# Performance work log

Measured on AMD Instinct MI355X. Metric: run time of the kernel, lower is better.

## Reference

```python
import jax, jax.numpy as jnp
import numpy as np

D_MODEL = 1024
B, S = 4, 4096


def setup_inputs() -> dict:
    key = jax.random.key(0)
    k1, k2, k3, k4, k5 = jax.random.split(key, 5)
    lim = 1.0 / np.sqrt(D_MODEL)  # nn.Linear default init range
    x = jax.random.normal(k1, (B, S, D_MODEL), dtype=jnp.float32)
    mask = jnp.ones((B, S), dtype=jnp.float32)
    W_up = jax.random.uniform(k2, (D_MODEL, D_MODEL), jnp.float32, -lim, lim)
    b_up = jax.random.uniform(k3, (D_MODEL,), jnp.float32, -lim, lim)
    W_f = jax.random.uniform(k4, (D_MODEL, D_MODEL), jnp.float32, -lim, lim)
    b_f = jax.random.uniform(k5, (D_MODEL,), jnp.float32, -lim, lim)
    decay_param = jnp.zeros((1,), dtype=jnp.float32)
    return {"x": x, "mask": mask, "W_up": W_up, "b_up": b_up,
            "W_f": W_f, "b_f": b_f, "decay_param": decay_param}


def _decay_scan(u, decay):
    # h_t = decay * h_{t-1} + u_t  along axis=1, via associative scan.
    # Element: (a, b) representing h -> a*h + b; compose: (a1*a2, b1*a2 + b2).
    a = jnp.broadcast_to(decay, u.shape)

    def combine(c1, c2):
        a1, b1 = c1
        a2, b2 = c2
        return a1 * a2, b1 * a2 + b2

    _, h = jax.lax.associative_scan(combine, (a, u), axis=1)
    return h


def reference(x, mask, W_up, b_up, W_f, b_f, decay_param):
    decay = jax.nn.sigmoid(decay_param)[0]
    # u_i = mask_i * linear_update(x_i)
    u = (jnp.einsum('bsd,ed->bse', x, W_up) + b_up) * mask[..., None]
    # h_t = sum_{i<=t} decay^(t-i) * u_i  (exponential-decay recurrence)
    h = _decay_scan(u, decay)
    return jnp.einsum('bsd,ed->bse', h, W_f) + b_f
```

## Files before the change

kernel.cpp:

```cpp
#include <hip/hip_runtime.h>
#include <hip/hip_bf16.h>
#include <cstdint>
#include <cstddef>

#define DMODEL 1024
#define BATCH  4
#define SEQ    4096
#define BSROWS (BATCH*SEQ)
#define CHUNK  32
#define NCHUNK (SEQ/CHUNK)
#define NCH_T  (BATCH*NCHUNK)

typedef __attribute__((ext_vector_type(8))) short bf16x8;
typedef __attribute__((ext_vector_type(4))) float f32x4;


__device__ __forceinline__ unsigned short f2bf(float f) {
  union { float f; uint32_t u; } v; v.f = f;
  uint32_t u = v.u;
  u += 0x7FFFu + ((u >> 16) & 1u);
  return (unsigned short)(u >> 16);
}

__device__ __forceinline__ float sigmoid_dev(const float* dp) {
  return 1.0f / (1.0f + expf(-dp[0]));
}

typedef __attribute__((address_space(1))) void void_g;
typedef __attribute__((address_space(3))) void void_l;

__device__ __forceinline__ void gl2lds16(const void* g, void* l) {
  __builtin_amdgcn_global_load_lds((void_g*)g, (void_l*)l, 16, 0, 0);
}

__device__ __forceinline__ void kloop64(
    const unsigned short* __restrict__ A, const unsigned short* __restrict__ B,
    int m0, int n0, f32x4 acc[2][2],
    unsigned short* As, unsigned short* Bs, int tid) {
  int lane = tid & 63, w = tid >> 6, wm = w & 1, wn = w >> 1;
  int quad = lane >> 4, l16 = lane & 15;
  int r = tid >> 3, cch = tid & 7;
  int g = cch ^ (r & 7);

  auto stage = [&](int t, int slot) {
    int k0 = t * 64;
    unsigned short* dA = As + slot * 4096;
    unsigned short* dB = Bs + slot * 4096;
    gl2lds16(A + (size_t)(m0 + r) * DMODEL + k0 + g * 8,      dA + r * 64 + cch * 8);
    gl2lds16(A + (size_t)(m0 + 32 + r) * DMODEL + k0 + g * 8, dA + (32 + r) * 64 + cch * 8);
    gl2lds16(B + (size_t)(n0 + r) * DMODEL + k0 + g * 8,      dB + r * 64 + cch * 8);
    gl2lds16(B + (size_t)(n0 + 32 + r) * DMODEL + k0 + g * 8, dB + (32 + r) * 64 + cch * 8);
  };
  auto compute = [&](int slot) {
    const bf16x8* Av = (const bf16x8*)(As + slot * 4096);
    const bf16x8* Bv = (const bf16x8*)(Bs + slot * 4096);
    #pragma unroll
    for (int kk = 0; kk < 2; ++kk) {
      bf16x8 af[2], bfr[2];
      #pragma unroll
      for (int i = 0; i < 2; ++i) {
        int rowA = wm * 32 + i * 16 + l16;
        af[i]  = Av[rowA * 8 + ((kk * 4 + quad) ^ (l16 & 7))];
        int rowB = wn * 32 + i * 16 + l16;
        bfr[i] = Bv[rowB * 8 + ((kk * 4 + quad) ^ (l16 & 7))];
      }
      __builtin_amdgcn_s_setprio(1);
      #pragma unroll
      for (int i = 0; i < 2; ++i)
        #pragma unroll
        for (int j = 0; j < 2; ++j)
          acc[i][j] = __builtin_amdgcn_mfma_f32_16x16x32_bf16(af[i], bfr[j], acc[i][j], 0, 0, 0);
      __builtin_amdgcn_s_setprio(0);
    }
  };

  stage(0, 0); stage(1, 1);
  asm volatile("s_waitcnt vmcnt(4)" ::: "memory");
  __builtin_amdgcn_s_barrier();
  asm volatile("" ::: "memory");
  int cur = 0;
  for (int t = 0; t < 14; ++t) {
    int ns = cur + 2; if (ns >= 3) ns -= 3;
    stage(t + 2, ns);
    compute(cur);
    asm volatile("s_waitcnt vmcnt(4)" ::: "memory");
    __builtin_amdgcn_s_barrier();
    asm volatile("" ::: "memory");
    cur = (cur == 2) ? 0 : cur + 1;
  }
  compute(cur);
  asm volatile("s_waitcnt vmcnt(0)" ::: "memory");
  __builtin_amdgcn_s_barrier();
  asm volatile("" ::: "memory");
  cur = (cur == 2) ? 0 : cur + 1;
  compute(cur);
}

__global__ __launch_bounds__(256) void prep_kernel(
    const float* __restrict__ x, const float* __restrict__ mask,
    const float* __restrict__ W_up, const float* __restrict__ b_up,
    const float* __restrict__ W_f, const float* __restrict__ dp,
    unsigned short* __restrict__ Wf_bf, unsigned short* __restrict__ WupT,
    float* __restrict__ bb, unsigned short* __restrict__ hv,
    float* __restrict__ carry, float* __restrict__ lbeta,
    float* __restrict__ cbeta) {
  __shared__ float tile[32][33];
  int blk = blockIdx.x;
  int tid = threadIdx.x;

  if (blk < 512) {
    float decay = sigmoid_dev(dp);
    int b = blk / NCHUNK, c = blk % NCHUNK;
    int base = b * SEQ + c * CHUNK;
    const float4* xp = (const float4*)(x + (size_t)base * DMODEL);
    const float4* mp4 = (const float4*)(mask + base);
    float mreg[32];
    #pragma unroll
    for (int q = 0; q < 8; ++q) {
      float4 t = mp4[q];
      mreg[q * 4 + 0] = t.x; mreg[q * 4 + 1] = t.y;
      mreg[q * 4 + 2] = t.z; mreg[q * 4 + 3] = t.w;
    }
    float4 h = make_float4(0.f, 0.f, 0.f, 0.f);
    #pragma unroll
    for (int s = 0; s < CHUNK; ++s) {
      float m = mreg[s];
      float4 xv = xp[(size_t)s * (DMODEL / 4) + tid];
      h.x = decay * h.x + m * xv.x;
      h.y = decay * h.y + m * xv.y;
      h.z = decay * h.z + m * xv.z;
      h.w = decay * h.w + m * xv.w;
      ushort4 o;
      o.x = f2bf(h.x); o.y = f2bf(h.y); o.z = f2bf(h.z); o.w = f2bf(h.w);
      ((ushort4*)hv)[(size_t)(base + s) * (DMODEL / 4) + tid] = o;
    }
    ((float4*)carry)[(size_t)blk * (DMODEL / 4) + tid] = h;
  } else if (blk < 1536) {
    int e = blk - 512;
    int lane = tid & 63, w = tid >> 6;
    float4 v = ((const float4*)(W_f + (size_t)e * DMODEL))[tid];
    float4 bu = ((const float4*)b_up)[tid];
    ushort4 o;
    o.x = f2bf(v.x); o.y = f2bf(v.y); o.z = f2bf(v.z); o.w = f2bf(v.w);
    ((ushort4*)(Wf_bf + (size_t)e * DMODEL))[tid] = o;
    float s = v.x * bu.x + v.y * bu.y + v.z * bu.z + v.w * bu.w;
    #pragma unroll
    for (int off = 32; off; off >>= 1) s += __shfl_down(s, off);
    if (lane == 0) ((float*)tile)[w] = s;
    __syncthreads();
    if (tid == 0)
      bb[e] = ((float*)tile)[0] + ((float*)tile)[1] +
              ((float*)tile)[2] + ((float*)tile)[3];
  } else if (blk < 2560) {
    int id = blk - 1536;
    int bx = id & 31, by = id >> 5;
    int tx = tid & 31, ty = tid >> 5;
    int xx = bx * 32 + tx;
    int y0 = by * 32;
    for (int j = ty; j < 32; j += 8)
      tile[j][tx] = W_up[(size_t)(y0 + j) * DMODEL + xx];
    __syncthreads();
    int dd = tid >> 3;
    int c4 = (tid & 7) * 4;
    ushort4 o;
    o.x = f2bf(tile[c4 + 0][dd]);
    o.y = f2bf(tile[c4 + 1][dd]);
    o.z = f2bf(tile[c4 + 2][dd]);
    o.w = f2bf(tile[c4 + 3][dd]);
    *(ushort4*)(WupT + (size_t)(bx * 32 + dd) * DMODEL + y0 + c4) = o;
  } else {
    float decay = sigmoid_dev(dp);
    int t = (blk - 2560) * 256 + tid;
    int s = t & 31;
    float h = mask[t];
    float wgt = decay;
    #pragma unroll
    for (int off = 1; off < 32; off <<= 1) {
      float up = __shfl_up(h, off);
      if (s >= off) h += wgt * up;
      wgt = wgt * wgt;
    }
    lbeta[t] = h;
    if (s == 31) cbeta[t >> 5] = h;
  }
}

__global__ __launch_bounds__(256) void mid2_kernel(
    const unsigned short* __restrict__ Wf_bf,
    const unsigned short* __restrict__ WupT,
    unsigned short* __restrict__ Wc,
    const float* __restrict__ carry, const float* __restrict__ cbeta,
    const float* __restrict__ dp,
    unsigned short* __restrict__ Pbf, float* __restrict__ pbeta) {
  __shared__ unsigned short As[3 * 64 * 64];
  __shared__ unsigned short Bs[3 * 64 * 64];
  int tid = threadIdx.x;
  if (blockIdx.x < 256) {
    int mt = blockIdx.x >> 4, nt = blockIdx.x & 15;
    f32x4 acc[2][2] = {};
    kloop64(Wf_bf, WupT, mt * 64, nt * 64, acc, As, Bs, tid);
    int lane = tid & 63, w = tid >> 6, wm = w & 1, wn = w >> 1;
    int quad = lane >> 4, l16 = lane & 15;
    #pragma unroll
    for (int j = 0; j < 2; ++j) {
      int col = nt * 64 + wn * 32 + j * 16 + l16;
      #pragma unroll
      for (int i = 0; i < 2; ++i) {
        int rowb = mt * 64 + wm * 32 + i * 16 + quad * 4;
        #pragma unroll
        for (int rr = 0; rr < 4; ++rr)
          Wc[(size_t)(rowb + rr) * DMODEL + col] = f2bf(acc[i][j][rr]);
      }
    }
  } else {
    float decay = sigmoid_dev(dp);
    float dL = powf(decay, (float)CHUNK);
    int gid = (blockIdx.x - 256) * 256 + tid;
    int b = gid >> 10, dd = gid & 1023;
    float P = 0.f;
    for (int c0 = 0; c0 < NCHUNK; c0 += 8) {
      float v[8];
      #pragma unroll
      for (int j = 0; j < 8; ++j)
        v[j] = carry[(size_t)(b * NCHUNK + c0 + j) * DMODEL + dd];
      #pragma unroll
      for (int j = 0; j < 8; ++j) {
        Pbf[(size_t)(b * NCHUNK + c0 + j) * DMODEL + dd] = f2bf(P);
        P = dL * P + v[j];
      }
    }
    if (dd == 0) {
      float Pb = 0.f;
      for (int c0 = 0; c0 < NCHUNK; c0 += 16) {
        float v[16];
        #pragma unroll
        for (int j = 0; j < 16; ++j) v[j] = cbeta[b * NCHUNK + c0 + j];
        #pragma unroll
        for (int j = 0; j < 16; ++j) {
          pbeta[b * NCHUNK + c0 + j] = Pb;
          Pb = dL * Pb + v[j];
        }
      }
    }
  }
}

__global__ __launch_bounds__(512) void gemm_main(
    const unsigned short* __restrict__ A,
    const unsigned short* __restrict__ Bm,
    const unsigned short* __restrict__ Pbf,
    const float* __restrict__ pbeta,
    const float* __restrict__ lbeta,
    const float* __restrict__ bb,
    const float* __restrict__ bias_f,
    const float* __restrict__ dp,
    float* __restrict__ out) {
  __shared__ unsigned short As[2 * 256 * 64];
  __shared__ unsigned short Bs[2 * 256 * 64];
  __shared__ unsigned short Ps[2 * 16 * 64];
  __shared__ float dpow[CHUNK];
  const int TSLOT = 256 * 64;
  const int PSLOT = 16 * 64;
  int tid = threadIdx.x;
  if (tid < CHUNK) {
    float decay = sigmoid_dev(dp);
    dpow[tid] = powf(decay, (float)(tid + 1));
  }

  int lane = tid & 63, wid = tid >> 6;
  int wm = wid >> 2, wn = wid & 3;
  int quad = lane >> 4, l16 = lane & 15;
  int r = tid >> 3, cch = tid & 7;
  int g = cch ^ (r & 7);

  int bid = blockIdx.x;
  int xcd = bid & 7, jb = bid >> 3;
  int m0 = (xcd * 8 + (jb >> 2)) * 256;
  int n0 = (jb & 3) * 256;
  int chunk0 = m0 >> 5;

  f32x4 acc[8][4] = {};
  f32x4 Pacc[4] = {};

  auto stageT = [&](int t, int p) {
    int k0 = t * 64;
    unsigned short* dA = As + p * TSLOT;
    unsigned short* dB = Bs + p * TSLOT;
    #pragma unroll
    for (int q = 0; q < 4; ++q)
      gl2lds16(A + (size_t)(m0 + q * 64 + r) * DMODEL + k0 + g * 8,
               dA + (q * 64 + r) * 64 + cch * 8);
    #pragma unroll
    for (int q = 0; q < 4; ++q)
      gl2lds16(Bm + (size_t)(n0 + q * 64 + r) * DMODEL + k0 + g * 8,
               dB + (q * 64 + r) * 64 + cch * 8);
    if (wid == 0) {
      int rp = lane >> 3, cp = lane & 7;
      int gp = cp ^ (rp & 7);
      gl2lds16(Pbf + (size_t)(chunk0 + rp) * DMODEL + k0 + gp * 8,
               Ps + p * PSLOT + lane * 8);
    }
  };
  auto compute = [&](int p) {
    const bf16x8* Av = (const bf16x8*)(As + p * TSLOT);
    const bf16x8* Bv = (const bf16x8*)(Bs + p * TSLOT);
    const bf16x8* Pv = (const bf16x8*)(Ps + p * PSLOT);
    #pragma unroll
    for (int kk = 0; kk < 2; ++kk) {
      bf16x8 bfr[4];
      #pragma unroll
      for (int j = 0; j < 4; ++j) {
        int rowB = wn * 64 + j * 16 + l16;
        bfr[j] = Bv[rowB * 8 + ((kk * 4 + quad) ^ (l16 & 7))];
      }
      bf16x8 pf = Pv[l16 * 8 + ((kk * 4 + quad) ^ (l16 & 7))];
      __builtin_amdgcn_s_setprio(1);
      #pragma unroll
      for (int j = 0; j < 4; ++j)
        Pacc[j] = __builtin_amdgcn_mfma_f32_16x16x32_bf16(pf, bfr[j], Pacc[j], 0, 0, 0);
      __builtin_amdgcn_s_setprio(0);
      #pragma unroll
      for (int i = 0; i < 8; ++i) {
        int rowA = wm * 128 + i * 16 + l16;
        bf16x8 af = Av[rowA * 8 + ((kk * 4 + quad) ^ (l16 & 7))];
        __builtin_amdgcn_s_setprio(1);
        #pragma unroll
        for (int j = 0; j < 4; ++j)
          acc[i][j] = __builtin_amdgcn_mfma_f32_16x16x32_bf16(af, bfr[j], acc[i][j], 0, 0, 0);
        __builtin_amdgcn_s_setprio(0);
      }
    }
  };

  stageT(0, 0);
  __syncthreads();

  for (int t = 0; t < 15; ++t) {
    int p = t & 1;
    stageT(t + 1, p ^ 1);
    compute(p);
    asm volatile("s_waitcnt vmcnt(0)" ::: "memory");
    __builtin_amdgcn_s_barrier();
    asm volatile("" ::: "memory");
  }
  compute(1);

  float* Plds = (float*)As;
  if (wm == 0 && quad < 2) {
    #pragma unroll
    for (int j = 0; j < 4; ++j)
      #pragma unroll
      for (int rr = 0; rr < 4; ++rr)
        Plds[(quad * 4 + rr) * 256 + wn * 64 + j * 16 + l16] = Pacc[j][rr];
  }
  __syncthreads();

  float bbv[4], bfv[4];
  #pragma unroll
  for (int j = 0; j < 4; ++j) {
    int col = n0 + wn * 64 + j * 16 + l16;
    bbv[j] = bb[col];
    bfv[j] = bias_f[col];
  }
  #pragma unroll
  for (int i = 0; i < 8; ++i) {
    int chl = wm * 4 + (i >> 1);
    float pb = pbeta[chunk0 + chl];
    #pragma unroll
    for (int rr = 0; rr < 4; ++rr) {
      int row = m0 + wm * 128 + i * 16 + quad * 4 + rr;
      float lb  = lbeta[row];
      float dpw = dpow[row & 31];
      float* outRow = out + (size_t)row * DMODEL;
      #pragma unroll
      for (int j = 0; j < 4; ++j) {
        int col = n0 + wn * 64 + j * 16 + l16;
        float po = Plds[chl * 256 + wn * 64 + j * 16 + l16] + pb * bbv[j];
        outRow[col] = acc[i][j][rr] + dpw * po + lb * bbv[j] + bfv[j];
      }
    }
  }
}


extern "C" void kernel_launch(void* const* d_in, const int* in_sizes, int n_in,
                              void* d_out, int out_size, void* d_ws, size_t ws_size,
                              hipStream_t stream) {
  const float* x    = (const float*)d_in[0];
  const float* mask = (const float*)d_in[1];
  const float* W_up = (const float*)d_in[2];
  const float* b_up = (const float*)d_in[3];
  const float* W_f  = (const float*)d_in[4];
  const float* b_f  = (const float*)d_in[5];
  const float* dp   = (const float*)d_in[6];
  float* out = (float*)d_out;

  char* ws = (char*)d_ws;
  unsigned short* hv    = (unsigned short*)(ws);
  unsigned short* Wc    = (unsigned short*)(ws + 33554432);
  unsigned short* Wf_bf = (unsigned short*)(ws + 35651584);
  unsigned short* WupT  = (unsigned short*)(ws + 37748736);
  float* carry  = (float*)(ws + 39845888);
  unsigned short* Pbf = (unsigned short*)(ws + 41943040);
  float* lbeta  = (float*)(ws + 45088768);
  float* cbeta  = (float*)(ws + 45154304);
  float* pbeta  = (float*)(ws + 45156352);
  float* bb     = (float*)(ws + 45158400);

  prep_kernel<<<2624, 256, 0, stream>>>(x, mask, W_up, b_up, W_f, dp,
                                        Wf_bf, WupT, bb, hv, carry, lbeta, cbeta);
  mid2_kernel<<<272, 256, 0, stream>>>(Wf_bf, WupT, Wc, carry, cbeta, dp,
                                       Pbf, pbeta);
  gemm_main<<<256, 512, 0, stream>>>(hv, Wc, Pbf, pbeta, lbeta, bb, b_f, dp, out);
}
```

Before: 185.3 us.

## Split prep kernel into scan and weight-prep kernels with x prefetch

The monolithic prep kernel is split into two launches. One handles the per-chunk decay scan and now computes the local beta prefix inline, removing the separate mask-scan blocks. The scan loop also software-prefetches x rows two steps ahead to keep more loads in flight. The W_f conversion now has each wave handle one row, which drops the shared-memory reduction and barrier; the cost is an extra kernel launch and a serial 32-step loop computing the beta values.

```diff
diff --git a/kernel.cpp b/kernel.cpp
--- a/kernel.cpp
+++ b/kernel.cpp
@@ -96,63 +96,88 @@
   compute(cur);
 }
 
-__global__ __launch_bounds__(256) void prep_kernel(
+__global__ __launch_bounds__(256) void prep_scan(
     const float* __restrict__ x, const float* __restrict__ mask,
+    const float* __restrict__ dp,
+    unsigned short* __restrict__ hv, float* __restrict__ carry,
+    float* __restrict__ lbeta, float* __restrict__ cbeta) {
+  int blk = blockIdx.x;
+  int tid = threadIdx.x;
+  float decay = sigmoid_dev(dp);
+  int b = blk / NCHUNK, c = blk % NCHUNK;
+  int base = b * SEQ + c * CHUNK;
+  const float4* xp = (const float4*)(x + (size_t)base * DMODEL);
+  const float4* mp4 = (const float4*)(mask + base);
+  float mreg[32];
+  #pragma unroll
+  for (int q = 0; q < 8; ++q) {
+    float4 t = mp4[q];
+    mreg[q * 4 + 0] = t.x; mreg[q * 4 + 1] = t.y;
+    mreg[q * 4 + 2] = t.z; mreg[q * 4 + 3] = t.w;
+  }
+
+  {
+    float hb = 0.f;
+    #pragma unroll
+    for (int i = 0; i < 32; ++i) {
+      float nv = decay * hb + mreg[i];
+      hb = (tid >= i) ? nv : hb;
+    }
+    if (tid < 32) {
+      lbeta[base + tid] = hb;
+      if (tid == 31) cbeta[base >> 5] = hb;
+    }
+  }
+
+  float4 x0 = xp[tid];
+  float4 x1 = xp[256 + tid];
+  float4 h = make_float4(0.f, 0.f, 0.f, 0.f);
+  #pragma unroll
+  for (int s = 0; s < CHUNK; ++s) {
+    float4 cur = x0;
+    x0 = x1;
+    if (s + 2 < CHUNK) x1 = xp[(size_t)(s + 2) * 256 + tid];
+    float m = mreg[s];
+    h.x = decay * h.x + m * cur.x;
+    h.y = decay * h.y + m * cur.y;
+    h.z = decay * h.z + m * cur.z;
+    h.w = decay * h.w + m * cur.w;
+    ushort4 o;
+    o.x = f2bf(h.x); o.y = f2bf(h.y); o.z = f2bf(h.z); o.w = f2bf(h.w);
+    ((ushort4*)hv)[(size_t)(base + s) * 256 + tid] = o;
+  }
+  ((float4*)carry)[(size_t)blk * 256 + tid] = h;
+}
+
+__global__ __launch_bounds__(256) void prep_misc(
     const float* __restrict__ W_up, const float* __restrict__ b_up,
-    const float* __restrict__ W_f, const float* __restrict__ dp,
+    const float* __restrict__ W_f,
     unsigned short* __restrict__ Wf_bf, unsigned short* __restrict__ WupT,
-    float* __restrict__ bb, unsigned short* __restrict__ hv,
-    float* __restrict__ carry, float* __restrict__ lbeta,
-    float* __restrict__ cbeta) {
+    float* __restrict__ bb) {
   __shared__ float tile[32][33];
   int blk = blockIdx.x;
   int tid = threadIdx.x;
-
-  if (blk < 512) {
-    float decay = sigmoid_dev(dp);
-    int b = blk / NCHUNK, c = blk % NCHUNK;
-    int base = b * SEQ + c * CHUNK;
-    const float4* xp = (const float4*)(x + (size_t)base * DMODEL);
-    const float4* mp4 = (const float4*)(mask + base);
-    float mreg[32];
-    #pragma unroll
-    for (int q = 0; q < 8; ++q) {
-      float4 t = mp4[q];
-      mreg[q * 4 + 0] = t.x; mreg[q * 4 + 1] = t.y;
-      mreg[q * 4 + 2] = t.z; mreg[q * 4 + 3] = t.w;
-    }
-    float4 h = make_float4(0.f, 0.f, 0.f, 0.f);
-    #pragma unroll
-    for (int s = 0; s < CHUNK; ++s) {
-      float m = mreg[s];
-      float4 xv = xp[(size_t)s * (DMODEL / 4) + tid];
-      h.x = decay * h.x + m * xv.x;
-      h.y = decay * h.y + m * xv.y;
-      h.z = decay * h.z + m * xv.z;
-      h.w = decay * h.w + m * xv.w;
+  if (blk < 256) {
+    int w = tid >> 6, lane = tid & 63;
+    int e = blk * 4 + w;
+    const float4* row4 = (const float4*)(W_f + (size_t)e * DMODEL);
+    const float4* bup4 = (const float4*)b_up;
+    ushort4* out4 = (ushort4*)(Wf_bf + (size_t)e * DMODEL);
+    float s = 0.f;
+    #pragma unroll
+    for (int q = 0; q < 4; ++q) {
+      float4 v  = row4[q * 64 + lane];
+      float4 bu = bup4[q * 64 + lane];
       ushort4 o;
-      o.x = f2bf(h.x); o.y = f2bf(h.y); o.z = f2bf(h.z); o.w = f2bf(h.w);
-      ((ushort4*)hv)[(size_t)(base + s) * (DMODEL / 4) + tid] = o;
-    }
-    ((float4*)carry)[(size_t)blk * (DMODEL / 4) + tid] = h;
-  } else if (blk < 1536) {
-    int e = blk - 512;
-    int lane = tid & 63, w = tid >> 6;
-    float4 v = ((const float4*)(W_f + (size_t)e * DMODEL))[tid];
-    float4 bu = ((const float4*)b_up)[tid];
-    ushort4 o;
-    o.x = f2bf(v.x); o.y = f2bf(v.y); o.z = f2bf(v.z); o.w = f2bf(v.w);
-    ((ushort4*)(Wf_bf + (size_t)e * DMODEL))[tid] = o;
-    float s = v.x * bu.x + v.y * bu.y + v.z * bu.z + v.w * bu.w;
+      o.x = f2bf(v.x); o.y = f2bf(v.y); o.z = f2bf(v.z); o.w = f2bf(v.w);
+      out4[q * 64 + lane] = o;
+      s += v.x * bu.x + v.y * bu.y + v.z * bu.z + v.w * bu.w;
+    }
     #pragma unroll
     for (int off = 32; off; off >>= 1) s += __shfl_down(s, off);
-    if (lane == 0) ((float*)tile)[w] = s;
-    __syncthreads();
-    if (tid == 0)
-      bb[e] = ((float*)tile)[0] + ((float*)tile)[1] +
-              ((float*)tile)[2] + ((float*)tile)[3];
-  } else if (blk < 2560) {
-    int id = blk - 1536;
+    if (lane == 0) bb[e] = s;
+  } else {
+    int id = blk - 256;
     int bx = id & 31, by = id >> 5;
     int tx = tid & 31, ty = tid >> 5;
     int xx = bx * 32 + tx;
@@ -168,20 +193,6 @@
     o.z = f2bf(tile[c4 + 2][dd]);
     o.w = f2bf(tile[c4 + 3][dd]);
     *(ushort4*)(WupT + (size_t)(bx * 32 + dd) * DMODEL + y0 + c4) = o;
-  } else {
-    float decay = sigmoid_dev(dp);
-    int t = (blk - 2560) * 256 + tid;
-    int s = t & 31;
-    float h = mask[t];
-    float wgt = decay;
-    #pragma unroll
-    for (int off = 1; off < 32; off <<= 1) {
-      float up = __shfl_up(h, off);
-      if (s >= off) h += wgt * up;
-      wgt = wgt * wgt;
-    }
-    lbeta[t] = h;
-    if (s == 31) cbeta[t >> 5] = h;
   }
 }
 
@@ -407,8 +418,8 @@
   float* pbeta  = (float*)(ws + 45156352);
   float* bb     = (float*)(ws + 45158400);
 
-  prep_kernel<<<2624, 256, 0, stream>>>(x, mask, W_up, b_up, W_f, dp,
-                                        Wf_bf, WupT, bb, hv, carry, lbeta, cbeta);
+  prep_scan<<<512, 256, 0, stream>>>(x, mask, dp, hv, carry, lbeta, cbeta);
+  prep_misc<<<1280, 256, 0, stream>>>(W_up, b_up, W_f, Wf_bf, WupT, bb);
   mid2_kernel<<<272, 256, 0, stream>>>(Wf_bf, WupT, Wc, carry, cbeta, dp,
                                        Pbf, pbeta);
   gemm_main<<<256, 512, 0, stream>>>(hv, Wc, Pbf, pbeta, lbeta, bb, b_f, dp, out);
```

Measured after the change: 188.1 us. Within noise of the previous version (+1.5%).
